# Optimization experiments

Hardware: AMD Instinct MI355X
Metric: run time of the kernel (lower is better)

Reference implementation:

```python
import jax, jax.numpy as jnp
import numpy as np

B, T, D, D_OUT = 8, 2048, 1024, 1024


def setup_inputs() -> dict:
    key = jax.random.key(0)
    k1, k2 = jax.random.split(key)
    x = jax.random.normal(k1, (B, T, D), dtype=jnp.float32)
    # dense projection params (Linear(D, D_OUT)); scaled init for stability
    W = jax.random.normal(k2, (D, D_OUT), dtype=jnp.float32) / np.sqrt(D)
    b = jnp.zeros((D_OUT,), dtype=jnp.float32)
    return {"x": x, "W": W, "b": b}


def reference(x, W, b):
    # x_: [B, T, D_OUT] projected tensor (self.dense(x))
    x_ = jnp.einsum("btd,de->bte", x, W) + b
    # correlation_matrix: [B, T, T], scaled by sqrt(d_out)
    scores = jnp.einsum("bte,bse->bts", x_, x_) / jnp.sqrt(jnp.asarray(D_OUT, x.dtype))
    # additive causal mask: -inf above the diagonal (triu, diagonal=1)
    causal = jnp.triu(jnp.full((T, T), -jnp.inf, dtype=x.dtype), k=1)
    scores = scores + causal
    # NOTE: original uses nn.Softmax(1) -> softmax over dim 1 (columns), not -1
    attn = jax.nn.softmax(scores, axis=1)
    # V is the RAW input x, not the projected x_
    return jnp.einsum("bts,bsd->btd", attn, x)
```

## Files before the change

### kernel.cpp

```cpp
#include <hip/hip_runtime.h>
#include <hip/hip_bf16.h>


#define B_ 8
#define T_ 2048
#define D_ 1024
#define E_ 1024
#define PIT 56

typedef unsigned short u16;
typedef __attribute__((ext_vector_type(8))) short short8;
typedef __attribute__((ext_vector_type(4))) float floatx4;

__device__ __forceinline__ float b2f(u16 u) {
    unsigned v = ((unsigned)u) << 16;
    float f; __builtin_memcpy(&f, &v, 4); return f;
}
__device__ __forceinline__ u16 f2b(float f) {
    unsigned v; __builtin_memcpy(&v, &f, 4);
    v = (v + 0x7FFFu + ((v >> 16) & 1u)) >> 16;
    return (u16)v;
}
__device__ __forceinline__ unsigned pkbf(float a, float b) {
    __hip_bfloat162 h = __float22bfloat162_rn(make_float2(a, b));
    unsigned u; __builtin_memcpy(&u, &h, 4); return u;
}

__device__ __forceinline__ void gl2lds16(const u16* gp, u16* lp) {
    __builtin_amdgcn_global_load_lds(
        (const __attribute__((address_space(1))) void*)(gp),
        (__attribute__((address_space(3))) void*)(lp), 16, 0, 0);
}

__device__ __forceinline__ void stage8(const u16* src, size_t srow, int kc,
                                       u16* lds, int wid, int lane)
{
    const int rl = lane >> 3, c = lane & 7;
    const int g = ((c ^ rl) << 3);
#pragma unroll
    for (int cc = 0; cc < 2; cc++) {
        const int r = cc * 64 + wid * 8;
        gl2lds16(src + (size_t)(r + rl) * srow + kc + g, &lds[r * 64]);
    }
}

__device__ __forceinline__ void gemm_step(const u16* As_, const u16* Bs_,
                                          int wr, int wc, int l15, int q, int sw,
                                          floatx4 (&acc)[2][4])
{
#pragma unroll
    for (int h = 0; h < 2; h++) {
        short8 a[2], b2[4];
#pragma unroll
        for (int i = 0; i < 2; i++)
            a[i] = *(const short8*)&As_[(wr + i * 16 + l15) * 64 + (((h * 4 + q) ^ sw) << 3)];
#pragma unroll
        for (int j = 0; j < 4; j++)
            b2[j] = *(const short8*)&Bs_[(wc + j * 16 + l15) * 64 + (((h * 4 + q) ^ sw) << 3)];
#pragma unroll
        for (int i = 0; i < 2; i++)
#pragma unroll
            for (int j = 0; j < 4; j++)
                acc[i][j] = __builtin_amdgcn_mfma_f32_16x16x32_bf16(a[i], b2[j], acc[i][j], 0, 0, 0);
    }
}

__device__ __forceinline__ float* mr_ptr(u16* S, int which, int b, int s) {
    const int row = which * 32 + b * 4 + (s >> 9);
    return (float*)(S + (size_t)row * T_ + 1024 + (s & 511) * 2);
}

__global__ __launch_bounds__(256) void k0_wt(const float* __restrict__ W,
                                             u16* __restrict__ WT)
{
    __shared__ float Ws[64 * 68];
    const int tid = threadIdx.x;
    const int k0 = blockIdx.x * 64, n0 = blockIdx.y * 64;
#pragma unroll
    for (int u = 0; u < 4; u++) {
        const int c = tid + 256 * u;
        const int row = c >> 4, c4 = c & 15;
        float4 v = *(const float4*)(W + (size_t)(k0 + row) * E_ + n0 + c4 * 4);
        *(float4*)&Ws[row * 68 + c4 * 4] = v;
    }
    __syncthreads();
#pragma unroll
    for (int u = 0; u < 2; u++) {
        const int c = tid + 256 * u;
        const int n = c >> 3, kc = c & 7;
        unsigned pk[4];
#pragma unroll
        for (int j = 0; j < 4; j++)
            pk[j] = pkbf(Ws[(kc * 8 + 2 * j) * 68 + n], Ws[(kc * 8 + 2 * j + 1) * 68 + n]);
        *(uint4*)(WT + (size_t)(n0 + n) * D_ + k0 + kc * 8) = make_uint4(pk[0], pk[1], pk[2], pk[3]);
    }
}

__global__ __launch_bounds__(256) void k00_xt(const float* __restrict__ x,
                                              u16* __restrict__ XT,
                                              u16* __restrict__ xbf,
                                              int do_xt)
{
    __shared__ float Xs[64 * 68];
    const int tid = threadIdx.x;
    const int s0 = blockIdx.x * 64, d0 = blockIdx.y * 64, b = blockIdx.z;
    const float* xb = x + (size_t)b * T_ * D_;
#pragma unroll
    for (int u = 0; u < 4; u++) {
        const int c = tid + 256 * u;
        const int row = c >> 4, c4 = c & 15;
        float4 v = *(const float4*)(xb + (size_t)(s0 + row) * D_ + d0 + c4 * 4);
        *(float4*)&Xs[row * 68 + c4 * 4] = v;
    }
    __syncthreads();
#pragma unroll
    for (int u = 0; u < 2; u++) {
        const int c = tid + 256 * u;
        const int row = c >> 3, off = c & 7;
        unsigned pk[4];
#pragma unroll
        for (int j = 0; j < 4; j++)
            pk[j] = pkbf(Xs[row * 68 + off * 8 + 2 * j], Xs[row * 68 + off * 8 + 2 * j + 1]);
        *(uint4*)(xbf + ((size_t)(b * T_ + s0 + row)) * D_ + d0 + off * 8) =
            make_uint4(pk[0], pk[1], pk[2], pk[3]);
    }
    if (!do_xt) return;
#pragma unroll
    for (int u = 0; u < 2; u++) {
        const int c = tid + 256 * u;
        const int d = c >> 3, sc = c & 7;
        unsigned pk[4];
#pragma unroll
        for (int j = 0; j < 4; j++)
            pk[j] = pkbf(Xs[(sc * 8 + 2 * j) * 68 + d], Xs[(sc * 8 + 2 * j + 1) * 68 + d]);
        *(uint4*)(XT + ((size_t)(b * D_ + d0 + d)) * T_ + s0 + sc * 8) =
            make_uint4(pk[0], pk[1], pk[2], pk[3]);
    }
}

__global__ __launch_bounds__(512, 4) void k1_proj(const u16* __restrict__ xbf,
                                                  const u16* __restrict__ WT,
                                                  const float* __restrict__ bias,
                                                  u16* __restrict__ y)
{
    __shared__ u16 As[2][128 * 64];
    __shared__ u16 Bs[2][128 * 64];
    const int tid = threadIdx.x;
    const int lane = tid & 63, wid = tid >> 6;
    const int wr = (wid >> 1) * 32, wc = (wid & 1) * 64;
    const int l15 = lane & 15, q = lane >> 4;
    const int sw = l15 & 7;
    const int lin = blockIdx.y * 8 + blockIdx.x;
    const int v = (lin & 7) * 128 + (lin >> 3);
    const int n0 = (v & 7) * 128, m0 = (v >> 3) * 128;
    const u16* Ab = xbf + (size_t)m0 * D_;
    const u16* Bb = WT + (size_t)n0 * D_;

    floatx4 acc[2][4];
#pragma unroll
    for (int i = 0; i < 2; i++)
#pragma unroll
        for (int j = 0; j < 4; j++) acc[i][j] = (floatx4){0.f, 0.f, 0.f, 0.f};

    stage8(Ab, D_, 0, As[0], wid, lane);
    stage8(Bb, D_, 0, Bs[0], wid, lane);
    __syncthreads();
    int cur = 0;
    for (int t = 0; t < 16; t++) {
        if (t + 1 < 16) {
            stage8(Ab, D_, (t + 1) * 64, As[cur ^ 1], wid, lane);
            stage8(Bb, D_, (t + 1) * 64, Bs[cur ^ 1], wid, lane);
        }
        gemm_step(As[cur], Bs[cur], wr, wc, l15, q, sw, acc);
        __syncthreads();
        cur ^= 1;
    }
    float bv[4];
#pragma unroll
    for (int j = 0; j < 4; j++) bv[j] = bias[n0 + wc + j * 16 + l15];
#pragma unroll
    for (int i = 0; i < 2; i++)
#pragma unroll
        for (int j = 0; j < 4; j++)
#pragma unroll
            for (int r = 0; r < 4; r++) {
                const int gm = m0 + wr + i * 16 + q * 4 + r;
                const int gn = n0 + wc + j * 16 + l15;
                y[(size_t)gm * E_ + gn] = f2b(acc[i][j][r] + bv[j]);
            }
}

__global__ __launch_bounds__(512, 4) void k2_score(const u16* __restrict__ y,
                                                   u16* __restrict__ S)
{
    __shared__ u16 As[2][128 * 64];
    __shared__ u16 Bs[2][128 * 64];
    const int tid = threadIdx.x;
    const int lane = tid & 63, wid = tid >> 6;
    const int wr = (wid >> 1) * 32, wc = (wid & 1) * 64;
    const int l15 = lane & 15, q = lane >> 4;
    const int sw = l15 & 7;
    const int lin = blockIdx.x;
    const int b = lin & 7;
    int idx = lin >> 3;
    int it = 0, base = 0;
    while (base + it + 1 <= idx) { base += it + 1; it++; }
    const int js = idx - base;
    const int t0 = it * 128, s0 = js * 128;
    const u16* yb = y + (size_t)b * T_ * E_;
    const u16* Ab = yb + (size_t)t0 * E_;
    const u16* Bb = yb + (size_t)s0 * E_;

    floatx4 acc[2][4];
#pragma unroll
    for (int i = 0; i < 2; i++)
#pragma unroll
        for (int j = 0; j < 4; j++) acc[i][j] = (floatx4){0.f, 0.f, 0.f, 0.f};

    stage8(Ab, E_, 0, As[0], wid, lane);
    stage8(Bb, E_, 0, Bs[0], wid, lane);
    __syncthreads();
    int cur = 0;
    for (int t = 0; t < 16; t++) {
        if (t + 1 < 16) {
            stage8(Ab, E_, (t + 1) * 64, As[cur ^ 1], wid, lane);
            stage8(Bb, E_, (t + 1) * 64, Bs[cur ^ 1], wid, lane);
        }
        gemm_step(As[cur], Bs[cur], wr, wc, l15, q, sw, acc);
        __syncthreads();
        cur ^= 1;
    }
#pragma unroll
    for (int i = 0; i < 2; i++)
#pragma unroll
        for (int j = 0; j < 4; j++)
#pragma unroll
            for (int r = 0; r < 4; r++) {
                const int t = t0 + wr + i * 16 + q * 4 + r;
                const int s = s0 + wc + j * 16 + l15;
                u16 o = (t < s) ? (u16)0xFF7F : f2b(acc[i][j][r] * 0.03125f);
                S[((size_t)(b * T_ + t)) * T_ + s] = o;
            }
}

__global__ __launch_bounds__(256) void k2b_stats(u16* __restrict__ S)
{
    __shared__ u16 St[64 * 64];
    __shared__ float sm[4][64], sz[4][64];
    const int tid = threadIdx.x;
    const int lane = tid & 63, w = tid >> 6;
    const int b = blockIdx.y;
    const int s0 = blockIdx.x * 64;
    const u16* Sb = S + (size_t)b * T_ * T_;
    float m = -3e38f, z = 0.f;
    for (int t0 = s0; t0 < T_; t0 += 64) {
        __syncthreads();
#pragma unroll
        for (int u = 0; u < 2; u++) {
            const int c = tid * 2 + u;
            const int row = c >> 3, off = c & 7;
            *(uint4*)&St[row * 64 + off * 8] =
                *(const uint4*)(Sb + (size_t)(t0 + row) * T_ + s0 + off * 8);
        }
        __syncthreads();
#pragma unroll
        for (int i = 0; i < 16; i++) {
            const float v = b2f(St[(w * 16 + i) * 64 + lane]);
            if (v > m) { z = z * __expf(m - v) + 1.f; m = v; }
            else z += __expf(v - m);
        }
    }
    sm[w][lane] = m; sz[w][lane] = z;
    __syncthreads();
    if (tid < 64) {
        float mm = sm[0][tid];
#pragma unroll
        for (int rr = 1; rr < 4; rr++) mm = fmaxf(mm, sm[rr][tid]);
        float zz = 0.f;
#pragma unroll
        for (int rr = 0; rr < 4; rr++) zz += sz[rr][tid] * __expf(sm[rr][tid] - mm);
        *mr_ptr(S, 0, b, s0 + tid) = mm;
        *mr_ptr(S, 1, b, s0 + tid) = 1.0f / zz;
    }
}

__global__ __launch_bounds__(256) void k3_pnorm(u16* __restrict__ S)
{
    const int row = blockIdx.x;
    const int b = row >> 11;
    const int t = row & (T_ - 1);
    const int sEnd = ((t >> 7) + 1) << 7;
    const int s0 = threadIdx.x * 8;
    if (s0 >= sEnd) return;
    u16* Sp = S + (size_t)row * T_ + s0;
    const float* mp = mr_ptr(S, 0, b, s0);
    const float* rp = mr_ptr(S, 1, b, s0);
    float mv[8], rv[8];
    *(float4*)&mv[0] = *(const float4*)mp;
    *(float4*)&mv[4] = *((const float4*)mp + 1);
    *(float4*)&rv[0] = *(const float4*)rp;
    *(float4*)&rv[4] = *((const float4*)rp + 1);
    ushort4 v0 = *(ushort4*)Sp;
    ushort4 v1 = *(ushort4*)(Sp + 4);
    u16 vv[8] = { v0.x, v0.y, v0.z, v0.w, v1.x, v1.y, v1.z, v1.w };
    u16 ov[8];
#pragma unroll
    for (int i = 0; i < 8; i++) {
        const int s = s0 + i;
        float p = 0.f;
        if (s <= t) p = __expf(b2f(vv[i]) - mv[i]) * rv[i];
        ov[i] = f2b(p);
    }
    *(ushort4*)Sp       = make_ushort4(ov[0], ov[1], ov[2], ov[3]);
    *(ushort4*)(Sp + 4) = make_ushort4(ov[4], ov[5], ov[6], ov[7]);
}

__global__ __launch_bounds__(512, 4) void k4_fast(const u16* __restrict__ P,
                                                  const u16* __restrict__ XT,
                                                  float* __restrict__ out)
{
    __shared__ u16 As[2][128 * 64];
    __shared__ u16 Bs[2][128 * 64];
    const int tid = threadIdx.x;
    const int lane = tid & 63, wid = tid >> 6;
    const int wr = (wid >> 1) * 32, wc = (wid & 1) * 64;
    const int l15 = lane & 15, q = lane >> 4;
    const int sw = l15 & 7;
    const int lin = blockIdx.x;
    const int b = lin & 7;
    const int r8 = lin >> 3;
    const int d0 = (r8 & 7) * 128;
    const int it = (T_ / 128 - 1) - (r8 >> 3);
    const int t0 = it * 128;
    const u16* Pb = P + (size_t)b * T_ * T_ + (size_t)t0 * T_;
    const u16* Xb = XT + (size_t)(b * D_ + d0) * T_;

    floatx4 acc[2][4];
#pragma unroll
    for (int i = 0; i < 2; i++)
#pragma unroll
        for (int j = 0; j < 4; j++) acc[i][j] = (floatx4){0.f, 0.f, 0.f, 0.f};

    const int nt = (it + 1) * 2;
    stage8(Pb, T_, 0, As[0], wid, lane);
    stage8(Xb, T_, 0, Bs[0], wid, lane);
    __syncthreads();
    int cur = 0;
    for (int t = 0; t < nt; t++) {
        if (t + 1 < nt) {
            stage8(Pb, T_, (t + 1) * 64, As[cur ^ 1], wid, lane);
            stage8(Xb, T_, (t + 1) * 64, Bs[cur ^ 1], wid, lane);
        }
        gemm_step(As[cur], Bs[cur], wr, wc, l15, q, sw, acc);
        __syncthreads();
        cur ^= 1;
    }
#pragma unroll
    for (int i = 0; i < 2; i++)
#pragma unroll
        for (int j = 0; j < 4; j++)
#pragma unroll
            for (int r = 0; r < 4; r++) {
                const int gt = t0 + wr + i * 16 + q * 4 + r;
                const int gd = d0 + wc + j * 16 + l15;
                out[(size_t)(b * T_ + gt) * D_ + gd] = acc[i][j][r];
            }
}

__global__ __launch_bounds__(256) void k4_fb(const u16* __restrict__ P,
                                             const float* __restrict__ x,
                                             float* __restrict__ out)
{
    __shared__ u16 As[128 * PIT];
    __shared__ u16 Bs[128 * PIT];
    const int tid = threadIdx.x;
    const int lane = tid & 63, wid = tid >> 6;
    const int wr = (wid >> 1) * 64, wc = (wid & 1) * 64;
    const int l15 = lane & 15, q = lane >> 4;
    const int it = (T_ / 128 - 1) - blockIdx.y;
    const int t0 = it * 128;
    const int d0 = blockIdx.x * 128;
    const int b = blockIdx.z;
    const u16* Pb = P + (size_t)b * T_ * T_;
    const float* xb = x + (size_t)b * T_ * D_;
    const int gn = tid & 127;
    const int kh0 = (tid >> 7) * 2;

    floatx4 acc[4][4];
#pragma unroll
    for (int i = 0; i < 4; i++)
#pragma unroll
        for (int j = 0; j < 4; j++) acc[i][j] = (floatx4){0.f, 0.f, 0.f, 0.f};

    const int kend = t0 + 128;
    for (int k0 = 0; k0 < kend; k0 += 32) {
        __syncthreads();
#pragma unroll
        for (int u = 0; u < 2; u++) {
            const int c = tid * 2 + u;
            const int row = c >> 2, off = c & 3;
            *(uint4*)&As[row * PIT + off * 8] =
                *(const uint4*)(Pb + (size_t)(t0 + row) * T_ + k0 + off * 8);
        }
#pragma unroll
        for (int u = 0; u < 2; u++) {
            const int kh = kh0 + u;
            float f[8];
#pragma unroll
            for (int j = 0; j < 8; j++)
                f[j] = xb[(size_t)(k0 + kh * 8 + j) * D_ + d0 + gn];
            uint4 pk = make_uint4(pkbf(f[0], f[1]), pkbf(f[2], f[3]),
                                  pkbf(f[4], f[5]), pkbf(f[6], f[7]));
            *(uint4*)&Bs[gn * PIT + kh * 8] = pk;
        }
        __syncthreads();
        short8 a[4], b2[4];
#pragma unroll
        for (int i = 0; i < 4; i++) a[i] = *(const short8*)&As[(wr + i * 16 + l15) * PIT + q * 8];
#pragma unroll
        for (int j = 0; j < 4; j++) b2[j] = *(const short8*)&Bs[(wc + j * 16 + l15) * PIT + q * 8];
#pragma unroll
        for (int i = 0; i < 4; i++)
#pragma unroll
            for (int j = 0; j < 4; j++)
                acc[i][j] = __builtin_amdgcn_mfma_f32_16x16x32_bf16(a[i], b2[j], acc[i][j], 0, 0, 0);
    }
#pragma unroll
    for (int i = 0; i < 4; i++)
#pragma unroll
        for (int j = 0; j < 4; j++)
#pragma unroll
            for (int r = 0; r < 4; r++) {
                const int gt = t0 + wr + i * 16 + q * 4 + r;
                const int gd = d0 + wc + j * 16 + l15;
                out[(size_t)(b * T_ + gt) * D_ + gd] = acc[i][j][r];
            }
}

extern "C" void kernel_launch(void* const* d_in, const int* in_sizes, int n_in,
                              void* d_out, int out_size, void* d_ws, size_t ws_size,
                              hipStream_t stream)
{
    const float* x    = (const float*)d_in[0];
    const float* W    = (const float*)d_in[1];
    const float* bias = (const float*)d_in[2];
    float* outf = (float*)d_out;
    u16*   y    = (u16*)d_out;
    u16*   WT   = y + ((size_t)1 << 24);
    u16*   S    = (u16*)d_ws;
    u16*   xbf  = S;
    u16*   XT   = S + ((size_t)1 << 25);
    const bool fast = ws_size >= ((size_t)96 << 20);

    dim3 g0(D_ / 64, E_ / 64);
    k0_wt<<<g0, 256, 0, stream>>>(W, WT);

    dim3 g00(T_ / 64, D_ / 64, B_);
    k00_xt<<<g00, 256, 0, stream>>>(x, XT, xbf, fast ? 1 : 0);

    dim3 g1(E_ / 128, (B_ * T_) / 128);
    k1_proj<<<g1, 512, 0, stream>>>(xbf, WT, bias, y);

    dim3 g2(136 * B_);
    k2_score<<<g2, 512, 0, stream>>>(y, S);

    dim3 g2b(T_ / 64, B_);
    k2b_stats<<<g2b, 256, 0, stream>>>(S);

    dim3 g3(B_ * T_);
    k3_pnorm<<<g3, 256, 0, stream>>>(S);

    dim3 g4((D_ / 128) * (T_ / 128) * B_);
    if (fast) k4_fast<<<g4, 512, 0, stream>>>(S, XT, outf);
    else {
        dim3 g4b(D_ / 128, T_ / 128, B_);
        k4_fb<<<g4b, 256, 0, stream>>>(S, x, outf);
    }
}
```

Before: 326.2 us.

## Split column softmax stats into row-chunked partial pass plus combine kernel

The column-wise softmax statistics kernel, which walked every row from the diagonal to the end serially with one block per column tile, is split into chunks of 256 rows across a new grid dimension. Each block loads its whole chunk into shared memory once, then runs a two-pass max-then-sum instead of the branchy online update. A small combine kernel merges the per-chunk max and sum into the final max and reciprocal. The aim is more parallelism and fewer exp calls and syncs, at the cost of an extra launch and a scratch area inside the S buffer.

Measured after the change: 294.3 us. 1.11x faster.

```diff
diff --git a/kernel.cpp b/kernel.cpp
--- a/kernel.cpp
+++ b/kernel.cpp
@@ -7,6 +7,8 @@
 #define D_ 1024
 #define E_ 1024
 #define PIT 56
+#define NCH 8
+#define CHR (T_ / NCH)
 
 typedef unsigned short u16;
 typedef __attribute__((ext_vector_type(8))) short short8;
@@ -67,6 +69,10 @@
 
 __device__ __forceinline__ float* mr_ptr(u16* S, int which, int b, int s) {
     const int row = which * 32 + b * 4 + (s >> 9);
+    return (float*)(S + (size_t)row * T_ + 1024 + (s & 511) * 2);
+}
+__device__ __forceinline__ float* part_ptr(u16* S, int which, int c, int b, int s) {
+    const int row = 64 + which * 256 + (c * 8 + b) * 4 + (s >> 9);
     return (float*)(S + (size_t)row * T_ + 1024 + (s & 511) * 2);
 }
 
@@ -243,34 +249,45 @@
             }
 }
 
-__global__ __launch_bounds__(256) void k2b_stats(u16* __restrict__ S)
-{
-    __shared__ u16 St[64 * 64];
+__global__ __launch_bounds__(256) void k2b_part(u16* __restrict__ S)
+{
+    __shared__ u16 St[CHR * 64];
     __shared__ float sm[4][64], sz[4][64];
     const int tid = threadIdx.x;
     const int lane = tid & 63, w = tid >> 6;
-    const int b = blockIdx.y;
     const int s0 = blockIdx.x * 64;
+    const int c  = blockIdx.y;
+    const int b  = blockIdx.z;
+    const int tb = max(c * CHR, s0);
+    const int te = (c + 1) * CHR;
+    if (tb >= te) return;
+    const int R = te - tb;
     const u16* Sb = S + (size_t)b * T_ * T_;
-    float m = -3e38f, z = 0.f;
-    for (int t0 = s0; t0 < T_; t0 += 64) {
-        __syncthreads();
-#pragma unroll
-        for (int u = 0; u < 2; u++) {
-            const int c = tid * 2 + u;
-            const int row = c >> 3, off = c & 7;
-            *(uint4*)&St[row * 64 + off * 8] =
-                *(const uint4*)(Sb + (size_t)(t0 + row) * T_ + s0 + off * 8);
-        }
-        __syncthreads();
-#pragma unroll
-        for (int i = 0; i < 16; i++) {
-            const float v = b2f(St[(w * 16 + i) * 64 + lane]);
-            if (v > m) { z = z * __expf(m - v) + 1.f; m = v; }
-            else z += __expf(v - m);
-        }
-    }
-    sm[w][lane] = m; sz[w][lane] = z;
+    for (int r0 = 0; r0 < R; r0 += 32) {
+        const int row = r0 + (tid >> 3), off = tid & 7;
+        *(uint4*)&St[row * 64 + off * 8] =
+            *(const uint4*)(Sb + (size_t)(tb + row) * T_ + s0 + off * 8);
+    }
+    __syncthreads();
+    const int rb = w * 64;
+    float m4[4] = {-3e38f, -3e38f, -3e38f, -3e38f};
+    float z4[4] = {0.f, 0.f, 0.f, 0.f};
+    float mt = -3e38f;
+    if (rb < R) {
+#pragma unroll 4
+        for (int i = 0; i < 64; i += 4)
+#pragma unroll
+            for (int j = 0; j < 4; j++)
+                m4[j] = fmaxf(m4[j], b2f(St[(rb + i + j) * 64 + lane]));
+        mt = fmaxf(fmaxf(m4[0], m4[1]), fmaxf(m4[2], m4[3]));
+#pragma unroll 4
+        for (int i = 0; i < 64; i += 4)
+#pragma unroll
+            for (int j = 0; j < 4; j++)
+                z4[j] += __expf(b2f(St[(rb + i + j) * 64 + lane]) - mt);
+    }
+    sm[w][lane] = mt;
+    sz[w][lane] = (z4[0] + z4[1]) + (z4[2] + z4[3]);
     __syncthreads();
     if (tid < 64) {
         float mm = sm[0][tid];
@@ -279,9 +296,24 @@
         float zz = 0.f;
 #pragma unroll
         for (int rr = 0; rr < 4; rr++) zz += sz[rr][tid] * __expf(sm[rr][tid] - mm);
-        *mr_ptr(S, 0, b, s0 + tid) = mm;
-        *mr_ptr(S, 1, b, s0 + tid) = 1.0f / zz;
-    }
+        *part_ptr(S, 0, c, b, s0 + tid) = mm;
+        *part_ptr(S, 1, c, b, s0 + tid) = zz;
+    }
+}
+
+__global__ __launch_bounds__(256) void k2c_comb(u16* __restrict__ S)
+{
+    const int s = blockIdx.x * 256 + threadIdx.x;
+    const int b = blockIdx.y;
+    float M = -3e38f, Z = 0.f;
+    for (int c = s >> 8; c < NCH; c++) {
+        const float mc = *part_ptr(S, 0, c, b, s);
+        const float zc = *part_ptr(S, 1, c, b, s);
+        if (mc > M) { Z = Z * __expf(M - mc) + zc; M = mc; }
+        else        { Z += zc * __expf(mc - M); }
+    }
+    *mr_ptr(S, 0, b, s) = M;
+    *mr_ptr(S, 1, b, s) = 1.0f / Z;
 }
 
 __global__ __launch_bounds__(256) void k3_pnorm(u16* __restrict__ S)
@@ -464,8 +496,11 @@
     dim3 g2(136 * B_);
     k2_score<<<g2, 512, 0, stream>>>(y, S);
 
-    dim3 g2b(T_ / 64, B_);
-    k2b_stats<<<g2b, 256, 0, stream>>>(S);
+    dim3 gp(T_ / 64, NCH, B_);
+    k2b_part<<<gp, 256, 0, stream>>>(S);
+
+    dim3 gc(T_ / 256, B_);
+    k2c_comb<<<gc, 256, 0, stream>>>(S);
 
     dim3 g3(B_ * T_);
     k3_pnorm<<<g3, 256, 0, stream>>>(S);
```

## Fuse column softmax statistics into score kernel with per-tile partials and combine pass

Applied to the files above, without the earlier changes.

The score GEMM epilogue now computes per-column partial max and sum-of-exp for each 128x128 tile, reducing them across lanes with shuffles and across waves in shared memory, and writes them into unused upper-triangle space of S. A small combine kernel then merges the per-row-tile partials into the final column max and reciprocal sum. This removes the separate stats pass, which re-read the whole lower-triangular score matrix. The score kernel gains extra exp work, shared memory and register pressure, and the partials must sit in S regions that nothing else overwrites.

Result: faster. 291.6 us (-10.6%).

```diff
diff --git a/kernel.cpp b/kernel.cpp
--- a/kernel.cpp
+++ b/kernel.cpp
@@ -68,6 +68,10 @@
 __device__ __forceinline__ float* mr_ptr(u16* S, int which, int b, int s) {
     const int row = which * 32 + b * 4 + (s >> 9);
     return (float*)(S + (size_t)row * T_ + 1024 + (s & 511) * 2);
+}
+__device__ __forceinline__ float2* part2_ptr(u16* S, int it, int b, int s) {
+    const int row = 64 + it * 8 + (s >> 8);
+    return (float2*)(S + (size_t)b * T_ * T_ + (size_t)row * T_ + 1024 + (s & 255) * 4);
 }
 
 __global__ __launch_bounds__(256) void k0_wt(const float* __restrict__ W,
@@ -195,6 +199,7 @@
 {
     __shared__ u16 As[2][128 * 64];
     __shared__ u16 Bs[2][128 * 64];
+    __shared__ float smf[8][64], smz[8][64];
     const int tid = threadIdx.x;
     const int lane = tid & 63, wid = tid >> 6;
     const int wr = (wid >> 1) * 32, wc = (wid & 1) * 64;
@@ -230,6 +235,9 @@
         __syncthreads();
         cur ^= 1;
     }
+    float pm[4] = {-1e38f, -1e38f, -1e38f, -1e38f};
+    float pz[4] = {0.f, 0.f, 0.f, 0.f};
+    u16 ov[2][4][4];
 #pragma unroll
     for (int i = 0; i < 2; i++)
 #pragma unroll
@@ -240,48 +248,66 @@
                 const int s = s0 + wc + j * 16 + l15;
                 u16 o = (t < s) ? (u16)0xFF7F : f2b(acc[i][j][r] * 0.03125f);
                 S[((size_t)(b * T_ + t)) * T_ + s] = o;
+                ov[i][j][r] = o;
+                if (t >= s) pm[j] = fmaxf(pm[j], b2f(o));
             }
-}
-
-__global__ __launch_bounds__(256) void k2b_stats(u16* __restrict__ S)
-{
-    __shared__ u16 St[64 * 64];
-    __shared__ float sm[4][64], sz[4][64];
-    const int tid = threadIdx.x;
-    const int lane = tid & 63, w = tid >> 6;
+#pragma unroll
+    for (int i = 0; i < 2; i++)
+#pragma unroll
+        for (int j = 0; j < 4; j++)
+#pragma unroll
+            for (int r = 0; r < 4; r++) {
+                const int t = t0 + wr + i * 16 + q * 4 + r;
+                const int s = s0 + wc + j * 16 + l15;
+                const float ez = __expf(b2f(ov[i][j][r]) - pm[j]);
+                pz[j] += (t >= s) ? ez : 0.f;
+            }
+#pragma unroll
+    for (int j = 0; j < 4; j++) {
+#pragma unroll
+        for (int d = 16; d < 64; d <<= 1) {
+            const float om = __shfl_xor(pm[j], d);
+            const float oz = __shfl_xor(pz[j], d);
+            const float nm = fmaxf(pm[j], om);
+            pz[j] = pz[j] * __expf(pm[j] - nm) + oz * __expf(om - nm);
+            pm[j] = nm;
+        }
+    }
+    if (q == 0)
+#pragma unroll
+        for (int j = 0; j < 4; j++) {
+            smf[wid][j * 16 + l15] = pm[j];
+            smz[wid][j * 16 + l15] = pz[j];
+        }
+    __syncthreads();
+    if (tid < 128) {
+        const int half = tid >> 6, cidx = tid & 63;
+        float M = -1e38f, Z = 0.f;
+#pragma unroll
+        for (int g = 0; g < 4; g++) {
+            const float m2 = smf[g * 2 + half][cidx];
+            const float z2 = smz[g * 2 + half][cidx];
+            const float nm = fmaxf(M, m2);
+            Z = Z * __expf(M - nm) + z2 * __expf(m2 - nm);
+            M = nm;
+        }
+        *part2_ptr(S, it, b, s0 + half * 64 + cidx) = make_float2(M, Z);
+    }
+}
+
+__global__ __launch_bounds__(256) void k2c_comb(u16* __restrict__ S)
+{
+    const int s = blockIdx.x * 256 + threadIdx.x;
     const int b = blockIdx.y;
-    const int s0 = blockIdx.x * 64;
-    const u16* Sb = S + (size_t)b * T_ * T_;
-    float m = -3e38f, z = 0.f;
-    for (int t0 = s0; t0 < T_; t0 += 64) {
-        __syncthreads();
-#pragma unroll
-        for (int u = 0; u < 2; u++) {
-            const int c = tid * 2 + u;
-            const int row = c >> 3, off = c & 7;
-            *(uint4*)&St[row * 64 + off * 8] =
-                *(const uint4*)(Sb + (size_t)(t0 + row) * T_ + s0 + off * 8);
-        }
-        __syncthreads();
-#pragma unroll
-        for (int i = 0; i < 16; i++) {
-            const float v = b2f(St[(w * 16 + i) * 64 + lane]);
-            if (v > m) { z = z * __expf(m - v) + 1.f; m = v; }
-            else z += __expf(v - m);
-        }
-    }
-    sm[w][lane] = m; sz[w][lane] = z;
-    __syncthreads();
-    if (tid < 64) {
-        float mm = sm[0][tid];
-#pragma unroll
-        for (int rr = 1; rr < 4; rr++) mm = fmaxf(mm, sm[rr][tid]);
-        float zz = 0.f;
-#pragma unroll
-        for (int rr = 0; rr < 4; rr++) zz += sz[rr][tid] * __expf(sm[rr][tid] - mm);
-        *mr_ptr(S, 0, b, s0 + tid) = mm;
-        *mr_ptr(S, 1, b, s0 + tid) = 1.0f / zz;
-    }
+    float M = -1e38f, Z = 0.f;
+    for (int it = s >> 7; it < 16; it++) {
+        const float2 p = *part2_ptr(S, it, b, s);
+        const float nm = fmaxf(M, p.x);
+        Z = Z * __expf(M - nm) + p.y * __expf(p.x - nm);
+        M = nm;
+    }
+    *mr_ptr(S, 0, b, s) = M;
+    *mr_ptr(S, 1, b, s) = 1.0f / Z;
 }
 
 __global__ __launch_bounds__(256) void k3_pnorm(u16* __restrict__ S)
@@ -464,8 +490,8 @@
     dim3 g2(136 * B_);
     k2_score<<<g2, 512, 0, stream>>>(y, S);
 
-    dim3 g2b(T_ / 64, B_);
-    k2b_stats<<<g2b, 256, 0, stream>>>(S);
+    dim3 gc(T_ / 256, B_);
+    k2c_comb<<<gc, 256, 0, stream>>>(S);
 
     dim3 g3(B_ * T_);
     k3_pnorm<<<g3, 256, 0, stream>>>(S);
```
